# Optimization experiments

Hardware: AMD Instinct MI355X
Metric: run time of the kernel (lower is better)

Reference implementation:

```python
import jax, jax.numpy as jnp
import numpy as np

N, L, S, H, D = 1, 4096, 4096, 8, 32


def setup_inputs() -> dict:
    key = jax.random.key(0)
    k1, k2, k3 = jax.random.split(key, 3)
    q = jax.random.normal(k1, (N, L, H, D), dtype=jnp.float32)
    k = jax.random.normal(k2, (N, S, H, D), dtype=jnp.float32)
    v = jax.random.normal(k3, (N, S, H, D), dtype=jnp.float32)
    q_mask = jnp.ones((N, L), dtype=bool)
    kv_mask = jnp.ones((N, S), dtype=bool)
    return {"q": q, "k": k, "v": v, "q_mask": q_mask, "kv_mask": kv_mask}


def reference(q, k, v, q_mask, kv_mask):
    # qk: [N, L, S, H] -- full score tensor as in the torch module
    qk = jnp.einsum('nlhd,nshd->nlsh', q, k)
    # mask BEFORE scaling (matches torch: masked_fill then divide by sqrt(D))
    mask = ~(q_mask[:, :, None, None] & kv_mask[:, None, :, None])
    qk = jnp.where(mask, jnp.float32(-1e9), qk)
    scale = q.shape[3] ** 0.5
    attn = jax.nn.softmax(qk / scale, axis=2)  # softmax over S
    out = jnp.einsum('nlsh,nshd->nlhd', attn, v)
    return out
```

## Files before the change

### kernel.cpp

```cpp
#include <hip/hip_runtime.h>
#include <hip/hip_bf16.h>

typedef __bf16 bf16x4 __attribute__((ext_vector_type(4)));
typedef __bf16 bf16x8 __attribute__((ext_vector_type(8)));
typedef float  f32x4  __attribute__((ext_vector_type(4)));
typedef float  f32x16 __attribute__((ext_vector_type(16)));

#define H_  8
#define D_  32
#define L_  4096
#define S_  4096
#define BM  64
#define BM4 128
#define BN  64
#define NSPLIT 4

static __device__ __forceinline__ f32x4 mfma_k16(bf16x4 a, bf16x4 b, f32x4 c) {
#if __has_builtin(__builtin_amdgcn_mfma_f32_16x16x16_bf16)
    return __builtin_amdgcn_mfma_f32_16x16x16_bf16(a, b, c, 0, 0, 0);
#else
    asm("v_mfma_f32_16x16x16_bf16 %0, %1, %2, %0" : "+v"(c) : "v"(a), "v"(b));
    return c;
#endif
}

__global__ __launch_bounds__(256)
void prep_k(const float* __restrict__ kk, __bf16* __restrict__ kb)
{
    const int oi = blockIdx.x * 256 + threadIdx.x;
    const int h    = oi >> 14;
    const int s    = (oi >> 2) & (S_ - 1);
    const int dseg = (oi & 3) * 8;
    const float* ip = kk + (((size_t)s * H_ + h) * D_ + dseg);
    float4 a = *(const float4*)ip, b = *(const float4*)(ip + 4);
    bf16x8 o;
    o[0]=(__bf16)a.x; o[1]=(__bf16)a.y; o[2]=(__bf16)a.z; o[3]=(__bf16)a.w;
    o[4]=(__bf16)b.x; o[5]=(__bf16)b.y; o[6]=(__bf16)b.z; o[7]=(__bf16)b.w;
    *(bf16x8*)(kb + ((size_t)h * S_ + s) * D_ + dseg) = o;
}

__global__ __launch_bounds__(256)
void prep_v(const float* __restrict__ v, __bf16* __restrict__ vt)
{
    const int h  = blockIdx.y;
    const int s0 = blockIdx.x * 64;
    __shared__ __bf16 T[D_][72];
    const int sr = threadIdx.x >> 2, dseg = (threadIdx.x & 3) * 8;
    const float* ip = v + (((size_t)(s0 + sr) * H_ + h) * D_ + dseg);
    float4 a = *(const float4*)ip, b = *(const float4*)(ip + 4);
    float vv[8] = {a.x, a.y, a.z, a.w, b.x, b.y, b.z, b.w};
#pragma unroll
    for (int j = 0; j < 8; ++j) T[dseg + j][sr] = (__bf16)vv[j];
    __syncthreads();
    const int d = threadIdx.x >> 3, so = (threadIdx.x & 7) * 8;
    bf16x8 o = *(const bf16x8*)(&T[d][so]);
    *(bf16x8*)(vt + ((size_t)h * D_ + d) * S_ + s0 + so) = o;
}

__global__ __launch_bounds__(256, 4)
void fattn_v4(const __bf16* __restrict__ kb, const __bf16* __restrict__ vtg,
              const float* __restrict__ q, float* __restrict__ num,
              float* __restrict__ den, int schunk)
{
    const int qt = blockIdx.x, h = blockIdx.y, sp = blockIdx.z;
    const int tid = threadIdx.x, wq = tid >> 6, lane = tid & 63;
    const int ln = lane & 31, hl = lane >> 5;

    __shared__ __align__(16) __bf16 Ks[2][64][40];
    __shared__ __align__(16) __bf16 Vt[2][D_][72];

    const float cs = 0.17677669529663687f * 1.4426950408889634f;

    const int qn = qt * BM4 + wq * 32 + ln;
    bf16x8 qf0, qf1;
    {
        const float* qp = q + ((size_t)qn * H_ + h) * D_ + hl * 8;
        float4 a = *(const float4*)qp,        b = *(const float4*)(qp + 4);
        float4 c = *(const float4*)(qp + 16), d = *(const float4*)(qp + 20);
        qf0[0]=(__bf16)(a.x*cs); qf0[1]=(__bf16)(a.y*cs);
        qf0[2]=(__bf16)(a.z*cs); qf0[3]=(__bf16)(a.w*cs);
        qf0[4]=(__bf16)(b.x*cs); qf0[5]=(__bf16)(b.y*cs);
        qf0[6]=(__bf16)(b.z*cs); qf0[7]=(__bf16)(b.w*cs);
        qf1[0]=(__bf16)(c.x*cs); qf1[1]=(__bf16)(c.y*cs);
        qf1[2]=(__bf16)(c.z*cs); qf1[3]=(__bf16)(c.w*cs);
        qf1[4]=(__bf16)(d.x*cs); qf1[5]=(__bf16)(d.y*cs);
        qf1[6]=(__bf16)(d.z*cs); qf1[7]=(__bf16)(d.w*cs);
    }

    f32x16 o = {0,0,0,0,0,0,0,0,0,0,0,0,0,0,0,0};
    const f32x16 z16 = {0,0,0,0,0,0,0,0,0,0,0,0,0,0,0,0};
    f32x4 accl = {0,0,0,0};

    const int srow = tid >> 2, kseg = (tid & 3) * 8;
    const int vd   = tid >> 3, vso  = (tid & 7) * 8;

    const int sbeg = sp * schunk;
    const int T = schunk / BN;

    const __bf16* kptr = kb  + ((size_t)h * S_ + sbeg + srow) * D_ + kseg;
    const __bf16* vptr = vtg + ((size_t)h * D_ + vd) * S_ + sbeg + vso;

    bf16x8 kf = *(const bf16x8*)kptr;
    bf16x8 vf = *(const bf16x8*)vptr;
    bf16x8 kn = kf, vn = vf;

    for (int t = 0; t < T; ++t) {
        const int b = t & 1;
        *(bf16x8*)(&Ks[b][srow][kseg]) = kf;
        *(bf16x8*)(&Vt[b][vd][vso])    = vf;
        if (t + 1 < T) {
            kn = *(const bf16x8*)(kptr + (size_t)(t + 1) * BN * D_);
            vn = *(const bf16x8*)(vptr + (t + 1) * BN);
        }
        __syncthreads();

#pragma unroll
        for (int sh = 0; sh < 2; ++sh) {
            bf16x8 ka0 = *(const bf16x8*)(&Ks[b][sh * 32 + ln][hl * 8]);
            bf16x8 ka1 = *(const bf16x8*)(&Ks[b][sh * 32 + ln][16 + hl * 8]);
            f32x16 st = __builtin_amdgcn_mfma_f32_32x32x16_bf16(ka0, qf0, z16, 0, 0, 0);
            st = __builtin_amdgcn_mfma_f32_32x32x16_bf16(ka1, qf1, st, 0, 0, 0);
            float p[16];
#pragma unroll
            for (int r = 0; r < 16; ++r) p[r] = __builtin_amdgcn_exp2f(st[r]);
            accl[0] += p[0]  + p[1]  + p[2]  + p[3];
            accl[1] += p[4]  + p[5]  + p[6]  + p[7];
            accl[2] += p[8]  + p[9]  + p[10] + p[11];
            accl[3] += p[12] + p[13] + p[14] + p[15];
#pragma unroll
            for (int u = 0; u < 2; ++u) {
                unsigned A, B, C, D;
                asm("v_cvt_pk_bf16_f32 %0, %1, %2" : "=v"(A) : "v"(p[u*8+0]), "v"(p[u*8+1]));
                asm("v_cvt_pk_bf16_f32 %0, %1, %2" : "=v"(B) : "v"(p[u*8+2]), "v"(p[u*8+3]));
                asm("v_cvt_pk_bf16_f32 %0, %1, %2" : "=v"(C) : "v"(p[u*8+4]), "v"(p[u*8+5]));
                asm("v_cvt_pk_bf16_f32 %0, %1, %2" : "=v"(D) : "v"(p[u*8+6]), "v"(p[u*8+7]));
                asm("v_permlane32_swap_b32 %0, %1" : "+v"(A), "+v"(C));
                asm("v_permlane32_swap_b32 %0, %1" : "+v"(B), "+v"(D));
                union { unsigned w[4]; bf16x8 f; } pb;
                pb.w[0] = A; pb.w[1] = B; pb.w[2] = C; pb.w[3] = D;
                const int slot = sh * 2 + u;
                bf16x8 va = *(const bf16x8*)(&Vt[b][ln][slot * 16 + hl * 8]);
                o = __builtin_amdgcn_mfma_f32_32x32x16_bf16(va, pb.f, o, 0, 0, 0);
            }
        }
        kf = kn; vf = vn;
    }

    float dsum = accl[0] + accl[1] + accl[2] + accl[3];
    dsum += __shfl_xor(dsum, 32, 64);

    float* pr = num + (((size_t)(sp * H_ + h) * L_ + qn) << 5);
    f32x4 w0 = {o[0],  o[1],  o[2],  o[3]};
    f32x4 w1 = {o[4],  o[5],  o[6],  o[7]};
    f32x4 w2 = {o[8],  o[9],  o[10], o[11]};
    f32x4 w3 = {o[12], o[13], o[14], o[15]};
    *(f32x4*)(pr      + hl * 4) = w0;
    *(f32x4*)(pr + 8  + hl * 4) = w1;
    *(f32x4*)(pr + 16 + hl * 4) = w2;
    *(f32x4*)(pr + 24 + hl * 4) = w3;
    if (hl == 0) den[(size_t)(sp * H_ + h) * L_ + qn] = dsum;
}

template<bool DIRECT>
__global__ __launch_bounds__(256, 6)
void fattn_main(const float* __restrict__ q, const float* __restrict__ kk,
                const float* __restrict__ v, float* __restrict__ num,
                float* __restrict__ den, float* __restrict__ out, int schunk)
{
    const int qt = blockIdx.x, h = blockIdx.y, sp = blockIdx.z;
    const int tid = threadIdx.x, wave = tid >> 6, lane = tid & 63;
    const int col = lane & 15, quad = lane >> 4;

    __shared__ __align__(16) __bf16 Ks[2][BN][40];
    __shared__ __align__(16) __bf16 Vt[2][D_][72];

    const float cs = 0.17677669529663687f * 1.4426950408889634f;

    const int qn = qt * BM + wave * 16 + col;
    bf16x8 qb;
    {
        const float* qp = q + ((size_t)qn * H_ + h) * D_ + quad * 8;
        float4 q0 = *(const float4*)qp;
        float4 q1 = *(const float4*)(qp + 4);
        qb[0]=(__bf16)(q0.x*cs); qb[1]=(__bf16)(q0.y*cs);
        qb[2]=(__bf16)(q0.z*cs); qb[3]=(__bf16)(q0.w*cs);
        qb[4]=(__bf16)(q1.x*cs); qb[5]=(__bf16)(q1.y*cs);
        qb[6]=(__bf16)(q1.z*cs); qb[7]=(__bf16)(q1.w*cs);
    }

    f32x4 o0 = {0,0,0,0}, o1 = {0,0,0,0}, accl = {0,0,0,0};
    const f32x4 zc = {0,0,0,0};
    const bf16x4 ones = {(__bf16)1.f, (__bf16)1.f, (__bf16)1.f, (__bf16)1.f};

    const int srow = tid >> 2;
    const int g    = tid & 3;
    const int dseg = g * 8;
    const int vcol = (srow + 16 * g) & 63;
    const int rot0 = (col >> 3) << 4;

    const int sbeg = sp * schunk;
    const int T = schunk / BN;

    float4 kf0, kf1, vf0, vf1;
    {
        const size_t goff = ((size_t)(sbeg + srow) * H_ + h) * D_ + dseg;
        kf0 = *(const float4*)(kk + goff);
        kf1 = *(const float4*)(kk + goff + 4);
        vf0 = *(const float4*)(v + goff);
        vf1 = *(const float4*)(v + goff + 4);
    }
    float4 kn0 = kf0, kn1 = kf1, vn0 = vf0, vn1 = vf1;

    for (int t = 0; t < T; ++t) {
        const int b = t & 1;
        {
            bf16x8 kb;
            kb[0]=(__bf16)kf0.x; kb[1]=(__bf16)kf0.y; kb[2]=(__bf16)kf0.z; kb[3]=(__bf16)kf0.w;
            kb[4]=(__bf16)kf1.x; kb[5]=(__bf16)kf1.y; kb[6]=(__bf16)kf1.z; kb[7]=(__bf16)kf1.w;
            *(bf16x8*)(&Ks[b][srow][dseg]) = kb;
            float vv[8] = {vf0.x, vf0.y, vf0.z, vf0.w, vf1.x, vf1.y, vf1.z, vf1.w};
#pragma unroll
            for (int j = 0; j < 8; ++j)
                Vt[b][dseg + j][vcol] = (__bf16)vv[j];
        }
        if (t + 1 < T) {
            const size_t goff = ((size_t)(sbeg + (t+1)*BN + srow) * H_ + h) * D_ + dseg;
            kn0 = *(const float4*)(kk + goff);
            kn1 = *(const float4*)(kk + goff + 4);
            vn0 = *(const float4*)(v + goff);
            vn1 = *(const float4*)(v + goff + 4);
        }
        __syncthreads();

#pragma unroll
        for (int sb = 0; sb < 4; ++sb) {
            bf16x8 ka = *(const bf16x8*)(&Ks[b][sb * 16 + col][quad * 8]);
            f32x4 st = __builtin_amdgcn_mfma_f32_16x16x32_bf16(ka, qb, zc, 0, 0, 0);
            bf16x4 pb;
#pragma unroll
            for (int r = 0; r < 4; ++r)
                pb[r] = (__bf16)__builtin_amdgcn_exp2f(st[r]);
            const int sc  = sb * 16 + quad * 4;
            bf16x4 va0 = *(const bf16x4*)(&Vt[b][col     ][(sc + rot0)      & 63]);
            bf16x4 va1 = *(const bf16x4*)(&Vt[b][col + 16][(sc + rot0 + 32) & 63]);
            o0   = mfma_k16(va0,  pb, o0);
            o1   = mfma_k16(va1,  pb, o1);
            accl = mfma_k16(ones, pb, accl);
        }
        kf0 = kn0; kf1 = kn1; vf0 = vn0; vf1 = vn1;
    }

    if (DIRECT) {
        const float inv = 1.f / accl[0];
        float* op = out + ((size_t)qn * H_ + h) * D_;
        f32x4 r0 = {o0[0]*inv, o0[1]*inv, o0[2]*inv, o0[3]*inv};
        f32x4 r1 = {o1[0]*inv, o1[1]*inv, o1[2]*inv, o1[3]*inv};
        *(f32x4*)(op + quad * 4)      = r0;
        *(f32x4*)(op + 16 + quad * 4) = r1;
    } else {
        float* pr = num + (((size_t)(sp * H_ + h) * L_ + qn) << 5);
        *(f32x4*)(pr + quad * 4)      = o0;
        *(f32x4*)(pr + 16 + quad * 4) = o1;
        if (quad == 0) den[(size_t)(sp * H_ + h) * L_ + qn] = accl[0];
    }
}

__global__ __launch_bounds__(256)
void fattn_combine(const float* __restrict__ num, const float* __restrict__ den,
                   float* __restrict__ out)
{
    const int i  = blockIdx.x * 256 + threadIdx.x;
    const int d4 = (i & 7) * 4;
    const int h  = (i >> 3) & 7;
    const int l  = i >> 6;
    f32x4 acc = {0,0,0,0};
    float dn = 0.f;
    for (int sp = 0; sp < NSPLIT; ++sp) {
        const float* pr = num + (((size_t)(sp * H_ + h) * L_ + l) << 5) + d4;
        f32x4 t = *(const f32x4*)pr;
        acc[0] += t[0]; acc[1] += t[1]; acc[2] += t[2]; acc[3] += t[3];
        dn += den[(size_t)(sp * H_ + h) * L_ + l];
    }
    const float inv = 1.f / dn;
    f32x4 r = {acc[0]*inv, acc[1]*inv, acc[2]*inv, acc[3]*inv};
    *(f32x4*)(out + ((size_t)l * H_ + h) * D_ + d4) = r;
}

extern "C" void kernel_launch(void* const* d_in, const int* in_sizes, int n_in,
                              void* d_out, int out_size, void* d_ws, size_t ws_size,
                              hipStream_t stream) {
    const float* q = (const float*)d_in[0];
    const float* k = (const float*)d_in[1];
    const float* v = (const float*)d_in[2];
    float* out = (float*)d_out;
    const size_t nnum = (size_t)NSPLIT * H_ * L_ * 32;
    const size_t nden = (size_t)NSPLIT * H_ * L_;
    const size_t nkv  = (size_t)H_ * S_ * D_;
    const size_t need_v4 = (nnum + nden) * sizeof(float) + 2 * nkv * sizeof(__bf16);
    if (ws_size >= need_v4) {
        float* num = (float*)d_ws;
        float* den = num + nnum;
        __bf16* kbp = (__bf16*)(den + nden);
        __bf16* vtp = kbp + nkv;
        prep_k<<<dim3((H_ * S_ * D_ / 8) / 256), 256, 0, stream>>>(k, kbp);
        prep_v<<<dim3(S_ / 64, H_), 256, 0, stream>>>(v, vtp);
        fattn_v4<<<dim3(L_ / BM4, H_, NSPLIT), 256, 0, stream>>>(
            kbp, vtp, q, num, den, S_ / NSPLIT);
        fattn_combine<<<dim3((L_ * H_ * D_ / 4) / 256), 256, 0, stream>>>(num, den, out);
    } else if (ws_size >= (nnum + nden) * sizeof(float)) {
        float* num = (float*)d_ws;
        float* den = num + nnum;
        fattn_main<false><<<dim3(L_ / BM, H_, NSPLIT), 256, 0, stream>>>(
            q, k, v, num, den, out, S_ / NSPLIT);
        fattn_combine<<<dim3((L_ * H_ * D_ / 4) / 256), 256, 0, stream>>>(num, den, out);
    } else {
        fattn_main<true><<<dim3(L_ / BM, H_, 1), 256, 0, stream>>>(
            q, k, v, nullptr, nullptr, out, S_);
    }
}
```

Before: 105.4 us.

## Merge K/V prep kernels and split attention waves across query and key halves

Merges the separate K-convert and V-transpose prep kernels into one launch. The attention kernel now arranges its 4 waves as 2 query groups by 2 key halves. Each wave handles 64 query rows over half of each 64-key tile, so its K and V fragments are read from LDS once and reused across two query subtiles. The two key-half partial results are then reduced through shared memory at the end. This cuts LDS fragment reads per MFMA and one launch, at the cost of more accumulator registers and an extra end-of-kernel reduction with barriers.

```diff
diff --git a/kernel.cpp b/kernel.cpp
--- a/kernel.cpp
+++ b/kernel.cpp
@@ -25,32 +25,28 @@
 }
 
 __global__ __launch_bounds__(256)
-void prep_k(const float* __restrict__ kk, __bf16* __restrict__ kb)
-{
-    const int oi = blockIdx.x * 256 + threadIdx.x;
-    const int h    = oi >> 14;
-    const int s    = (oi >> 2) & (S_ - 1);
-    const int dseg = (oi & 3) * 8;
-    const float* ip = kk + (((size_t)s * H_ + h) * D_ + dseg);
-    float4 a = *(const float4*)ip, b = *(const float4*)(ip + 4);
-    bf16x8 o;
-    o[0]=(__bf16)a.x; o[1]=(__bf16)a.y; o[2]=(__bf16)a.z; o[3]=(__bf16)a.w;
-    o[4]=(__bf16)b.x; o[5]=(__bf16)b.y; o[6]=(__bf16)b.z; o[7]=(__bf16)b.w;
-    *(bf16x8*)(kb + ((size_t)h * S_ + s) * D_ + dseg) = o;
-}
-
-__global__ __launch_bounds__(256)
-void prep_v(const float* __restrict__ v, __bf16* __restrict__ vt)
+void prep_kv(const float* __restrict__ kk, const float* __restrict__ v,
+             __bf16* __restrict__ kb, __bf16* __restrict__ vt)
 {
     const int h  = blockIdx.y;
     const int s0 = blockIdx.x * 64;
+    const int sr = threadIdx.x >> 2, dseg = (threadIdx.x & 3) * 8;
+    {
+        const float* ip = kk + (((size_t)(s0 + sr) * H_ + h) * D_ + dseg);
+        float4 a = *(const float4*)ip, b = *(const float4*)(ip + 4);
+        bf16x8 o;
+        o[0]=(__bf16)a.x; o[1]=(__bf16)a.y; o[2]=(__bf16)a.z; o[3]=(__bf16)a.w;
+        o[4]=(__bf16)b.x; o[5]=(__bf16)b.y; o[6]=(__bf16)b.z; o[7]=(__bf16)b.w;
+        *(bf16x8*)(kb + ((size_t)h * S_ + s0 + sr) * D_ + dseg) = o;
+    }
     __shared__ __bf16 T[D_][72];
-    const int sr = threadIdx.x >> 2, dseg = (threadIdx.x & 3) * 8;
-    const float* ip = v + (((size_t)(s0 + sr) * H_ + h) * D_ + dseg);
-    float4 a = *(const float4*)ip, b = *(const float4*)(ip + 4);
-    float vv[8] = {a.x, a.y, a.z, a.w, b.x, b.y, b.z, b.w};
-#pragma unroll
-    for (int j = 0; j < 8; ++j) T[dseg + j][sr] = (__bf16)vv[j];
+    {
+        const float* ip = v + (((size_t)(s0 + sr) * H_ + h) * D_ + dseg);
+        float4 a = *(const float4*)ip, b = *(const float4*)(ip + 4);
+        float vv[8] = {a.x, a.y, a.z, a.w, b.x, b.y, b.z, b.w};
+#pragma unroll
+        for (int j = 0; j < 8; ++j) T[dseg + j][sr] = (__bf16)vv[j];
+    }
     __syncthreads();
     const int d = threadIdx.x >> 3, so = (threadIdx.x & 7) * 8;
     bf16x8 o = *(const bf16x8*)(&T[d][so]);
@@ -58,38 +54,44 @@
 }
 
 __global__ __launch_bounds__(256, 4)
-void fattn_v4(const __bf16* __restrict__ kb, const __bf16* __restrict__ vtg,
+void fattn_v5(const __bf16* __restrict__ kb, const __bf16* __restrict__ vtg,
               const float* __restrict__ q, float* __restrict__ num,
               float* __restrict__ den, int schunk)
 {
     const int qt = blockIdx.x, h = blockIdx.y, sp = blockIdx.z;
-    const int tid = threadIdx.x, wq = tid >> 6, lane = tid & 63;
+    const int tid = threadIdx.x, wave = tid >> 6, lane = tid & 63;
     const int ln = lane & 31, hl = lane >> 5;
+    const int wq = wave >> 1, ws = wave & 1;
 
     __shared__ __align__(16) __bf16 Ks[2][64][40];
     __shared__ __align__(16) __bf16 Vt[2][D_][72];
 
     const float cs = 0.17677669529663687f * 1.4426950408889634f;
 
-    const int qn = qt * BM4 + wq * 32 + ln;
-    bf16x8 qf0, qf1;
-    {
+    bf16x8 qf[2][2];
+#pragma unroll
+    for (int qh = 0; qh < 2; ++qh) {
+        const int qn = qt * BM4 + wq * 64 + qh * 32 + ln;
         const float* qp = q + ((size_t)qn * H_ + h) * D_ + hl * 8;
-        float4 a = *(const float4*)qp,        b = *(const float4*)(qp + 4);
-        float4 c = *(const float4*)(qp + 16), d = *(const float4*)(qp + 20);
-        qf0[0]=(__bf16)(a.x*cs); qf0[1]=(__bf16)(a.y*cs);
-        qf0[2]=(__bf16)(a.z*cs); qf0[3]=(__bf16)(a.w*cs);
-        qf0[4]=(__bf16)(b.x*cs); qf0[5]=(__bf16)(b.y*cs);
-        qf0[6]=(__bf16)(b.z*cs); qf0[7]=(__bf16)(b.w*cs);
-        qf1[0]=(__bf16)(c.x*cs); qf1[1]=(__bf16)(c.y*cs);
-        qf1[2]=(__bf16)(c.z*cs); qf1[3]=(__bf16)(c.w*cs);
-        qf1[4]=(__bf16)(d.x*cs); qf1[5]=(__bf16)(d.y*cs);
-        qf1[6]=(__bf16)(d.z*cs); qf1[7]=(__bf16)(d.w*cs);
-    }
-
-    f32x16 o = {0,0,0,0,0,0,0,0,0,0,0,0,0,0,0,0};
+        float4 a = *(const float4*)qp,        b2 = *(const float4*)(qp + 4);
+        float4 c = *(const float4*)(qp + 16), d2 = *(const float4*)(qp + 20);
+        qf[qh][0][0]=(__bf16)(a.x*cs);  qf[qh][0][1]=(__bf16)(a.y*cs);
+        qf[qh][0][2]=(__bf16)(a.z*cs);  qf[qh][0][3]=(__bf16)(a.w*cs);
+        qf[qh][0][4]=(__bf16)(b2.x*cs); qf[qh][0][5]=(__bf16)(b2.y*cs);
+        qf[qh][0][6]=(__bf16)(b2.z*cs); qf[qh][0][7]=(__bf16)(b2.w*cs);
+        qf[qh][1][0]=(__bf16)(c.x*cs);  qf[qh][1][1]=(__bf16)(c.y*cs);
+        qf[qh][1][2]=(__bf16)(c.z*cs);  qf[qh][1][3]=(__bf16)(c.w*cs);
+        qf[qh][1][4]=(__bf16)(d2.x*cs); qf[qh][1][5]=(__bf16)(d2.y*cs);
+        qf[qh][1][6]=(__bf16)(d2.z*cs); qf[qh][1][7]=(__bf16)(d2.w*cs);
+    }
+
+    f32x16 o[2];
+    o[0] = (f32x16){0,0,0,0,0,0,0,0,0,0,0,0,0,0,0,0};
+    o[1] = (f32x16){0,0,0,0,0,0,0,0,0,0,0,0,0,0,0,0};
     const f32x16 z16 = {0,0,0,0,0,0,0,0,0,0,0,0,0,0,0,0};
-    f32x4 accl = {0,0,0,0};
+    f32x4 accl[2];
+    accl[0] = (f32x4){0,0,0,0};
+    accl[1] = (f32x4){0,0,0,0};
 
     const int srow = tid >> 2, kseg = (tid & 3) * 8;
     const int vd   = tid >> 3, vso  = (tid & 7) * 8;
@@ -114,19 +116,22 @@
         }
         __syncthreads();
 
-#pragma unroll
-        for (int sh = 0; sh < 2; ++sh) {
-            bf16x8 ka0 = *(const bf16x8*)(&Ks[b][sh * 32 + ln][hl * 8]);
-            bf16x8 ka1 = *(const bf16x8*)(&Ks[b][sh * 32 + ln][16 + hl * 8]);
-            f32x16 st = __builtin_amdgcn_mfma_f32_32x32x16_bf16(ka0, qf0, z16, 0, 0, 0);
-            st = __builtin_amdgcn_mfma_f32_32x32x16_bf16(ka1, qf1, st, 0, 0, 0);
+        bf16x8 ka0 = *(const bf16x8*)(&Ks[b][ws * 32 + ln][hl * 8]);
+        bf16x8 ka1 = *(const bf16x8*)(&Ks[b][ws * 32 + ln][16 + hl * 8]);
+        bf16x8 va0 = *(const bf16x8*)(&Vt[b][ln][ws * 32 + hl * 8]);
+        bf16x8 va1 = *(const bf16x8*)(&Vt[b][ln][ws * 32 + 16 + hl * 8]);
+
+#pragma unroll
+        for (int qh = 0; qh < 2; ++qh) {
+            f32x16 st = __builtin_amdgcn_mfma_f32_32x32x16_bf16(ka0, qf[qh][0], z16, 0, 0, 0);
+            st = __builtin_amdgcn_mfma_f32_32x32x16_bf16(ka1, qf[qh][1], st, 0, 0, 0);
             float p[16];
 #pragma unroll
             for (int r = 0; r < 16; ++r) p[r] = __builtin_amdgcn_exp2f(st[r]);
-            accl[0] += p[0]  + p[1]  + p[2]  + p[3];
-            accl[1] += p[4]  + p[5]  + p[6]  + p[7];
-            accl[2] += p[8]  + p[9]  + p[10] + p[11];
-            accl[3] += p[12] + p[13] + p[14] + p[15];
+            accl[qh][0] += p[0]  + p[1]  + p[2]  + p[3];
+            accl[qh][1] += p[4]  + p[5]  + p[6]  + p[7];
+            accl[qh][2] += p[8]  + p[9]  + p[10] + p[11];
+            accl[qh][3] += p[12] + p[13] + p[14] + p[15];
 #pragma unroll
             for (int u = 0; u < 2; ++u) {
                 unsigned A, B, C, D;
@@ -138,27 +143,52 @@
                 asm("v_permlane32_swap_b32 %0, %1" : "+v"(B), "+v"(D));
                 union { unsigned w[4]; bf16x8 f; } pb;
                 pb.w[0] = A; pb.w[1] = B; pb.w[2] = C; pb.w[3] = D;
-                const int slot = sh * 2 + u;
-                bf16x8 va = *(const bf16x8*)(&Vt[b][ln][slot * 16 + hl * 8]);
-                o = __builtin_amdgcn_mfma_f32_32x32x16_bf16(va, pb.f, o, 0, 0, 0);
+                o[qh] = __builtin_amdgcn_mfma_f32_32x32x16_bf16(u ? va1 : va0, pb.f, o[qh], 0, 0, 0);
             }
         }
         kf = kn; vf = vn;
     }
 
-    float dsum = accl[0] + accl[1] + accl[2] + accl[3];
-    dsum += __shfl_xor(dsum, 32, 64);
-
-    float* pr = num + (((size_t)(sp * H_ + h) * L_ + qn) << 5);
-    f32x4 w0 = {o[0],  o[1],  o[2],  o[3]};
-    f32x4 w1 = {o[4],  o[5],  o[6],  o[7]};
-    f32x4 w2 = {o[8],  o[9],  o[10], o[11]};
-    f32x4 w3 = {o[12], o[13], o[14], o[15]};
-    *(f32x4*)(pr      + hl * 4) = w0;
-    *(f32x4*)(pr + 8  + hl * 4) = w1;
-    *(f32x4*)(pr + 16 + hl * 4) = w2;
-    *(f32x4*)(pr + 24 + hl * 4) = w3;
-    if (hl == 0) den[(size_t)(sp * H_ + h) * L_ + qn] = dsum;
+    float dsum[2];
+#pragma unroll
+    for (int qh = 0; qh < 2; ++qh) {
+        float s4 = accl[qh][0] + accl[qh][1] + accl[qh][2] + accl[qh][3];
+        s4 += __shfl_xor(s4, 32, 64);
+        dsum[qh] = s4;
+    }
+
+    __syncthreads();
+    float* rb = (wq == 0) ? (float*)&Ks[0][0][0] : (float*)&Vt[0][0][0];
+    if (ws == 1) {
+#pragma unroll
+        for (int qh = 0; qh < 2; ++qh) {
+#pragma unroll
+            for (int r = 0; r < 16; ++r)
+                rb[(qh * 16 + r) * 64 + lane] = o[qh][r];
+            rb[2048 + qh * 64 + lane] = dsum[qh];
+        }
+    }
+    __syncthreads();
+    if (ws == 0) {
+#pragma unroll
+        for (int qh = 0; qh < 2; ++qh) {
+#pragma unroll
+            for (int r = 0; r < 16; ++r)
+                o[qh][r] += rb[(qh * 16 + r) * 64 + lane];
+            dsum[qh] += rb[2048 + qh * 64 + lane];
+            const int qn = qt * BM4 + wq * 64 + qh * 32 + ln;
+            float* pr = num + (((size_t)(sp * H_ + h) * L_ + qn) << 5);
+            f32x4 w0 = {o[qh][0],  o[qh][1],  o[qh][2],  o[qh][3]};
+            f32x4 w1 = {o[qh][4],  o[qh][5],  o[qh][6],  o[qh][7]};
+            f32x4 w2 = {o[qh][8],  o[qh][9],  o[qh][10], o[qh][11]};
+            f32x4 w3 = {o[qh][12], o[qh][13], o[qh][14], o[qh][15]};
+            *(f32x4*)(pr      + hl * 4) = w0;
+            *(f32x4*)(pr + 8  + hl * 4) = w1;
+            *(f32x4*)(pr + 16 + hl * 4) = w2;
+            *(f32x4*)(pr + 24 + hl * 4) = w3;
+            if (hl == 0) den[(size_t)(sp * H_ + h) * L_ + qn] = dsum[qh];
+        }
+    }
 }
 
 template<bool DIRECT>
@@ -296,15 +326,14 @@
     const size_t nnum = (size_t)NSPLIT * H_ * L_ * 32;
     const size_t nden = (size_t)NSPLIT * H_ * L_;
     const size_t nkv  = (size_t)H_ * S_ * D_;
-    const size_t need_v4 = (nnum + nden) * sizeof(float) + 2 * nkv * sizeof(__bf16);
-    if (ws_size >= need_v4) {
+    const size_t need_v5 = (nnum + nden) * sizeof(float) + 2 * nkv * sizeof(__bf16);
+    if (ws_size >= need_v5) {
         float* num = (float*)d_ws;
         float* den = num + nnum;
         __bf16* kbp = (__bf16*)(den + nden);
         __bf16* vtp = kbp + nkv;
-        prep_k<<<dim3((H_ * S_ * D_ / 8) / 256), 256, 0, stream>>>(k, kbp);
-        prep_v<<<dim3(S_ / 64, H_), 256, 0, stream>>>(v, vtp);
-        fattn_v4<<<dim3(L_ / BM4, H_, NSPLIT), 256, 0, stream>>>(
+        prep_kv<<<dim3(S_ / 64, H_), 256, 0, stream>>>(k, v, kbp, vtp);
+        fattn_v5<<<dim3(L_ / BM4, H_, NSPLIT), 256, 0, stream>>>(
             kbp, vtp, q, num, den, S_ / NSPLIT);
         fattn_combine<<<dim3((L_ * H_ * D_ / 4) / 256), 256, 0, stream>>>(num, den, out);
     } else if (ws_size >= (nnum + nden) * sizeof(float)) {
```

New measurement: 104.2 us. About the same (-1.2%).
